# Performance work log

Measured on AMD Instinct MI355X. Metric: run time of the kernel, lower is better.

Reference implementation:

```python
import jax, jax.numpy as jnp
import numpy as np

N_QUBITS = 8
INV_SQRT2 = 1.0 / np.sqrt(2.0).astype(np.float32)


def _vqc(q_in, qw):
    """Statevector simulation of the PennyLane circuit.
    q_in: (B, n) real angles; qw: (2, n) trainable rotation params.
    Circuit: H on all wires -> AngleEmbedding (RX(q_in)) -> RY(qw[0]), RZ(qw[1])
    per wire -> CNOT ring -> expval(PauliZ) per wire. Returns (B, n) real.
    """
    B, n = q_in.shape
    # Per-qubit single-qubit chain applied to |0>: v = RZ @ RY @ RX @ H |0>
    half = q_in * 0.5
    cx, sx = jnp.cos(half), jnp.sin(half)
    u = (cx - 1j * sx) * INV_SQRT2          # RX(x) @ H|0> = u * (1, 1)
    ay, az = qw[0] * 0.5, qw[1] * 0.5       # (n,)
    cy, sy = jnp.cos(ay), jnp.sin(ay)
    v0 = jnp.exp(-1j * az) * (cy - sy) * u  # (B, n)
    v1 = jnp.exp(1j * az) * (cy + sy) * u
    v = jnp.stack([v0, v1], axis=-1)        # (B, n, 2) complex per-qubit states
    # Tensor-product state over n qubits (n small, loop is over qubit count)
    state = v[:, 0]
    for w in range(1, n):
        state = (state[:, :, None] * v[:, w][:, None, :]).reshape(B, -1)
    state = state.reshape((B,) + (2,) * n)

    def cnot(s, c, t):
        s = jnp.moveaxis(s, (1 + c, 1 + t), (1, 2))
        s = jnp.stack([s[:, 0], jnp.flip(s[:, 1], axis=1)], axis=1)
        return jnp.moveaxis(s, (1, 2), (1 + c, 1 + t))

    for i in range(n - 1):
        state = cnot(state, i, i + 1)
    state = cnot(state, n - 1, 0)

    probs = (state.real ** 2 + state.imag ** 2).reshape(B, -1)  # (B, 2^n)
    z = []
    for w in range(n):
        p = probs.reshape(B, 2 ** w, 2, -1)
        z.append(p[:, :, 0].sum(axis=(1, 2)) - p[:, :, 1].sum(axis=(1, 2)))
    return jnp.stack(z, axis=-1)  # (B, n)


def reference(x, embed, Wi, bi, qw, Wo, bo, fcW, fcb):
    # padding_idx=0: row 0 of the embedding is zero
    emb_tab = embed.at[0].set(0.0)
    emb = emb_tab[x]                         # (B, T, E)
    B, T, E = emb.shape
    H = Wo.shape[1]

    def step(carry, x_t):                    # x_t: (B, E)
        h, c = carry
        comb = jnp.concatenate([x_t, h], axis=-1)          # (B, E+H)
        # 4 gates fused: (4, nq, E+H) x (B, E+H) -> (4, B, nq)
        q_in = jnp.pi * jnp.tanh(jnp.einsum('gqd,bd->gbq', Wi, comb) + bi[:, None, :])
        q_feat = jax.vmap(_vqc)(q_in, qw)                  # (4, B, nq)
        gates = jnp.einsum('ghq,gbq->gbh', Wo, q_feat) + bo[:, None, :]  # (4, B, H)
        f = jax.nn.sigmoid(gates[0])
        i = jax.nn.sigmoid(gates[1])
        g = jnp.tanh(gates[2])
        o = jax.nn.sigmoid(gates[3])
        c_new = f * c + i * g
        h_new = o * jnp.tanh(c_new)
        return (h_new, c_new), h_new

    h0 = jnp.zeros((B, H), emb.dtype)
    c0 = jnp.zeros((B, H), emb.dtype)
    _, hs = jax.lax.scan(step, (h0, c0), jnp.moveaxis(emb, 1, 0))  # hs: (T, B, H)
    H_seq = jnp.moveaxis(hs, 0, 1)                                  # (B, T, H)

    mask = (x != 0).astype(emb.dtype)[..., None]                    # (B, T, 1)
    pooled = (H_seq * mask).sum(axis=1) / (mask.sum(axis=1) + 1e-9)
    # dropout is identity in eval mode
    return pooled @ fcW.T + fcb


def setup_inputs() -> dict:
    key = jax.random.key(0)
    ks = jax.random.split(key, 9)
    B, T, E, H, NQ, V, C = 1024, 128, 128, 256, N_QUBITS, 38, 2
    return {
        'x': jax.random.randint(ks[0], (B, T), 0, V),
        'embed': jax.random.normal(ks[1], (V, E), jnp.float32),
        'Wi': jax.random.normal(ks[2], (4, NQ, E + H), jnp.float32) * (1.0 / np.sqrt(E + H)),
        'bi': jax.random.normal(ks[3], (4, NQ), jnp.float32) * 0.01,
        'qw': jax.random.normal(ks[4], (4, 2, NQ), jnp.float32),
        'Wo': jax.random.normal(ks[5], (4, H, NQ), jnp.float32) * (1.0 / np.sqrt(NQ)),
        'bo': jax.random.normal(ks[6], (4, H), jnp.float32) * 0.01,
        'fcW': jax.random.normal(ks[7], (C, H), jnp.float32) * (1.0 / np.sqrt(H)),
        'fcb': jax.random.normal(ks[8], (C,), jnp.float32) * 0.01,
    }
```

## Files before the change

kernel.cpp:

```cpp
#include <hip/hip_runtime.h>
#include <math.h>


__device__ __forceinline__ float sigmoidf_(float v) { return 1.0f / (1.0f + expf(-v)); }

__global__ __launch_bounds__(256) void qlstm_stab(
    const float* __restrict__ qw,
    const float* __restrict__ Wo,
    const float* __restrict__ bo,
    const float* __restrict__ fcW,
    float* __restrict__ s_tab)
{
  __shared__ float feat[4][8];
  __shared__ float red[8];
  const int t = blockIdx.x;
  const int h = threadIdx.x;

  if (h < 4) {
    const int g = h;
    float z[8];
#pragma unroll
    for (int j = 0; j < 8; ++j) z[j] = -sinf(qw[g * 16 + j]);
    float p = z[1];
#pragma unroll
    for (int j = 2; j < 8; ++j) p *= z[j];
    feat[g][0] = p;
    p = z[0];
#pragma unroll
    for (int w = 1; w < 8; ++w) { p *= z[w]; feat[g][w] = p; }
  }
  __syncthreads();

  float gate[4];
#pragma unroll
  for (int g = 0; g < 4; ++g) {
    const float* wrow = Wo + ((g << 8) + h) * 8;
    float acc = bo[(g << 8) + h];
#pragma unroll
    for (int q = 0; q < 8; ++q) acc += wrow[q] * feat[g][q];
    gate[g] = acc;
  }
  const float f  = sigmoidf_(gate[0]);
  const float ii = sigmoidf_(gate[1]);
  const float gg = tanhf(gate[2]);
  const float o  = sigmoidf_(gate[3]);
  const float S  = ii * gg;

  float c = 0.0f;
  for (int k = 0; k <= t; ++k) c = f * c + S;
  const float ht = o * tanhf(c);

  float p0 = fcW[h]       * ht;
  float p1 = fcW[256 + h] * ht;
#pragma unroll
  for (int off = 32; off > 0; off >>= 1) {
    p0 += __shfl_down(p0, off);
    p1 += __shfl_down(p1, off);
  }
  const int lane = h & 63, wv = h >> 6;
  if (lane == 0) { red[wv * 2] = p0; red[wv * 2 + 1] = p1; }
  __syncthreads();
  if (h == 0) {
    s_tab[t * 2 + 0] = red[0] + red[2] + red[4] + red[6];
    s_tab[t * 2 + 1] = red[1] + red[3] + red[5] + red[7];
  }
}

__global__ __launch_bounds__(256) void qlstm_pool(
    const int* __restrict__ x,
    const float* __restrict__ s_tab,
    const float* __restrict__ fcb,
    float* __restrict__ out)
{
  __shared__ float ss[256];
  const int tid = threadIdx.x;
  ss[tid] = s_tab[tid];
  __syncthreads();

  const int lane = tid & 63, wv = tid >> 6;
  const int b = (blockIdx.x << 2) + wv;
  const int* xb = x + b * 128;

  const int t0 = lane, t1 = lane + 64;
  const int m0 = (xb[t0] != 0) ? 1 : 0;
  const int m1 = (xb[t1] != 0) ? 1 : 0;
  float cnt = (float)(m0 + m1);
  float a0 = 0.0f, a1 = 0.0f;
  if (m0) { a0 += ss[t0 * 2]; a1 += ss[t0 * 2 + 1]; }
  if (m1) { a0 += ss[t1 * 2]; a1 += ss[t1 * 2 + 1]; }

#pragma unroll
  for (int off = 32; off > 0; off >>= 1) {
    cnt += __shfl_down(cnt, off);
    a0  += __shfl_down(a0, off);
    a1  += __shfl_down(a1, off);
  }
  if (lane == 0) {
    const float inv = 1.0f / (cnt + 1e-9f);
    out[b * 2 + 0] = a0 * inv + fcb[0];
    out[b * 2 + 1] = a1 * inv + fcb[1];
  }
}

extern "C" void kernel_launch(void* const* d_in, const int* in_sizes, int n_in,
                              void* d_out, int out_size, void* d_ws, size_t ws_size,
                              hipStream_t stream) {
  const int*   x    = (const int*)  d_in[0];
  const float* qw   = (const float*)d_in[4];
  const float* Wo   = (const float*)d_in[5];
  const float* bo   = (const float*)d_in[6];
  const float* fcW  = (const float*)d_in[7];
  const float* fcb  = (const float*)d_in[8];
  float* out = (float*)d_out;
  float* s_tab = (float*)d_ws;

  const int T = 128;
  const int B = in_sizes[0] / T;

  qlstm_stab<<<T, 256, 0, stream>>>(qw, Wo, bo, fcW, s_tab);
  qlstm_pool<<<B / 4, 256, 0, stream>>>(x, s_tab, fcb, out);
}
```

Before: 72.93 us.

## Fuse step-table and pooling kernels, recomputing the table per block

Merges the per-timestep projection kernel and the masked-pooling kernel into one launch. Each block now rebuilds the 128-entry projected hidden-state table in shared memory: every wave takes 32 timesteps, runs the cell recurrence for four hidden units per lane, and reduces with shuffles. This removes the second launch and the global workspace round trip. In exchange, every block redundantly recomputes the whole table, and the last wave's serial recurrence runs up to 128 steps.

```diff
diff --git a/kernel.cpp b/kernel.cpp
--- a/kernel.cpp
+++ b/kernel.cpp
@@ -4,20 +4,23 @@
 
 __device__ __forceinline__ float sigmoidf_(float v) { return 1.0f / (1.0f + expf(-v)); }
 
-__global__ __launch_bounds__(256) void qlstm_stab(
+__global__ __launch_bounds__(256) void qlstm_fused(
+    const int* __restrict__ x,
     const float* __restrict__ qw,
     const float* __restrict__ Wo,
     const float* __restrict__ bo,
     const float* __restrict__ fcW,
-    float* __restrict__ s_tab)
+    const float* __restrict__ fcb,
+    float* __restrict__ out)
 {
   __shared__ float feat[4][8];
-  __shared__ float red[8];
-  const int t = blockIdx.x;
-  const int h = threadIdx.x;
+  __shared__ float ss[128][2];
+  const int tid  = threadIdx.x;
+  const int lane = tid & 63;
+  const int wv   = tid >> 6;
 
-  if (h < 4) {
-    const int g = h;
+  if (tid < 4) {
+    const int g = tid;
     float z[8];
 #pragma unroll
     for (int j = 0; j < 8; ++j) z[j] = -sinf(qw[g * 16 + j]);
@@ -31,63 +34,59 @@
   }
   __syncthreads();
 
-  float gate[4];
+  float f_[4], S_[4], o_[4], w0_[4], w1_[4];
 #pragma unroll
-  for (int g = 0; g < 4; ++g) {
-    const float* wrow = Wo + ((g << 8) + h) * 8;
-    float acc = bo[(g << 8) + h];
+  for (int k = 0; k < 4; ++k) {
+    const int h = lane + (k << 6);
+    float gate[4];
 #pragma unroll
-    for (int q = 0; q < 8; ++q) acc += wrow[q] * feat[g][q];
-    gate[g] = acc;
+    for (int g = 0; g < 4; ++g) {
+      const float* wrow = Wo + ((g << 8) + h) * 8;
+      float acc = bo[(g << 8) + h];
+#pragma unroll
+      for (int q = 0; q < 8; ++q) acc += wrow[q] * feat[g][q];
+      gate[g] = acc;
+    }
+    const float f  = sigmoidf_(gate[0]);
+    const float ii = sigmoidf_(gate[1]);
+    const float gg = tanhf(gate[2]);
+    const float o  = sigmoidf_(gate[3]);
+    f_[k] = f; S_[k] = ii * gg; o_[k] = o;
+    w0_[k] = fcW[h]; w1_[k] = fcW[256 + h];
   }
-  const float f  = sigmoidf_(gate[0]);
-  const float ii = sigmoidf_(gate[1]);
-  const float gg = tanhf(gate[2]);
-  const float o  = sigmoidf_(gate[3]);
-  const float S  = ii * gg;
 
-  float c = 0.0f;
-  for (int k = 0; k <= t; ++k) c = f * c + S;
-  const float ht = o * tanhf(c);
-
-  float p0 = fcW[h]       * ht;
-  float p1 = fcW[256 + h] * ht;
+  float c_[4] = {0.f, 0.f, 0.f, 0.f};
+  const int t_lo = wv << 5, t_hi = t_lo + 32;
+  for (int t = 0; t < t_hi; ++t) {
 #pragma unroll
-  for (int off = 32; off > 0; off >>= 1) {
-    p0 += __shfl_down(p0, off);
-    p1 += __shfl_down(p1, off);
+    for (int k = 0; k < 4; ++k) c_[k] = f_[k] * c_[k] + S_[k];
+    if (t >= t_lo) {
+      float q0 = 0.f, q1 = 0.f;
+#pragma unroll
+      for (int k = 0; k < 4; ++k) {
+        const float ht = o_[k] * tanhf(c_[k]);
+        q0 += w0_[k] * ht;
+        q1 += w1_[k] * ht;
+      }
+#pragma unroll
+      for (int off = 32; off > 0; off >>= 1) {
+        q0 += __shfl_down(q0, off);
+        q1 += __shfl_down(q1, off);
+      }
+      if (lane == 0) { ss[t][0] = q0; ss[t][1] = q1; }
+    }
   }
-  const int lane = h & 63, wv = h >> 6;
-  if (lane == 0) { red[wv * 2] = p0; red[wv * 2 + 1] = p1; }
-  __syncthreads();
-  if (h == 0) {
-    s_tab[t * 2 + 0] = red[0] + red[2] + red[4] + red[6];
-    s_tab[t * 2 + 1] = red[1] + red[3] + red[5] + red[7];
-  }
-}
-
-__global__ __launch_bounds__(256) void qlstm_pool(
-    const int* __restrict__ x,
-    const float* __restrict__ s_tab,
-    const float* __restrict__ fcb,
-    float* __restrict__ out)
-{
-  __shared__ float ss[256];
-  const int tid = threadIdx.x;
-  ss[tid] = s_tab[tid];
   __syncthreads();
 
-  const int lane = tid & 63, wv = tid >> 6;
   const int b = (blockIdx.x << 2) + wv;
   const int* xb = x + b * 128;
-
   const int t0 = lane, t1 = lane + 64;
   const int m0 = (xb[t0] != 0) ? 1 : 0;
   const int m1 = (xb[t1] != 0) ? 1 : 0;
   float cnt = (float)(m0 + m1);
-  float a0 = 0.0f, a1 = 0.0f;
-  if (m0) { a0 += ss[t0 * 2]; a1 += ss[t0 * 2 + 1]; }
-  if (m1) { a0 += ss[t1 * 2]; a1 += ss[t1 * 2 + 1]; }
+  float a0 = 0.f, a1 = 0.f;
+  if (m0) { a0 += ss[t0][0]; a1 += ss[t0][1]; }
+  if (m1) { a0 += ss[t1][0]; a1 += ss[t1][1]; }
 
 #pragma unroll
   for (int off = 32; off > 0; off >>= 1) {
@@ -105,18 +104,16 @@
 extern "C" void kernel_launch(void* const* d_in, const int* in_sizes, int n_in,
                               void* d_out, int out_size, void* d_ws, size_t ws_size,
                               hipStream_t stream) {
-  const int*   x    = (const int*)  d_in[0];
-  const float* qw   = (const float*)d_in[4];
-  const float* Wo   = (const float*)d_in[5];
-  const float* bo   = (const float*)d_in[6];
-  const float* fcW  = (const float*)d_in[7];
-  const float* fcb  = (const float*)d_in[8];
+  const int*   x   = (const int*)  d_in[0];
+  const float* qw  = (const float*)d_in[4];
+  const float* Wo  = (const float*)d_in[5];
+  const float* bo  = (const float*)d_in[6];
+  const float* fcW = (const float*)d_in[7];
+  const float* fcb = (const float*)d_in[8];
   float* out = (float*)d_out;
-  float* s_tab = (float*)d_ws;
 
   const int T = 128;
   const int B = in_sizes[0] / T;
 
-  qlstm_stab<<<T, 256, 0, stream>>>(qw, Wo, bo, fcW, s_tab);
-  qlstm_pool<<<B / 4, 256, 0, stream>>>(x, s_tab, fcb, out);
+  qlstm_fused<<<B / 4, 256, 0, stream>>>(x, qw, Wo, bo, fcW, fcb, out);
 }
```

New measurement: 94.65 us. +29.8%, slower.
